# Kernel optimization log

Measured on AMD Instinct MI355X. Metric: run time of the kernel, lower is better.

The kernel has to match this reference:

```python
import jax, jax.numpy as jnp
import numpy as np

B, S, H, D = 4, 2048, 12, 64
HIDDEN = H * D  # 768
WINDOW = 64     # config.local_attention // 2
ROPE_THETA = 10000.0  # local_rope_theta for sliding layers


def rotate_half(x):
    d = x.shape[-1] // 2
    return jnp.concatenate([-x[..., d:], x[..., :d]], axis=-1)


def setup_inputs() -> dict:
    key = jax.random.key(0)
    k1, k2, k3 = jax.random.split(key, 3)
    hidden_states = jax.random.normal(k1, (B, S, HIDDEN), dtype=jnp.float32)
    # RoPE tables (HF style): inv_freq over half dims, duplicated
    inv_freq = 1.0 / (ROPE_THETA ** (jnp.arange(0, D, 2, dtype=jnp.float32) / D))  # [D/2]
    pos = jnp.arange(S, dtype=jnp.float32)
    freqs = pos[:, None] * inv_freq[None, :]          # [S, D/2]
    emb = jnp.concatenate([freqs, freqs], axis=-1)    # [S, D]
    cos = jnp.broadcast_to(jnp.cos(emb)[None], (B, S, D))
    sin = jnp.broadcast_to(jnp.sin(emb)[None], (B, S, D))
    # sliding-window additive mask [B,1,S,S]
    idx = jnp.arange(S)
    allowed = jnp.abs(idx[:, None] - idx[None, :]) <= WINDOW
    neg = jnp.finfo(jnp.float32).min
    attention_mask = jnp.broadcast_to(
        jnp.where(allowed, 0.0, neg)[None, None], (B, 1, S, S)
    ).astype(jnp.float32)
    std = 0.02
    Wqkv_w = jax.random.normal(k2, (3 * HIDDEN, HIDDEN), dtype=jnp.float32) * std
    Wo_w = jax.random.normal(k3, (HIDDEN, HIDDEN), dtype=jnp.float32) * std
    return {"hidden_states": hidden_states, "cos": cos, "sin": sin,
            "attention_mask": attention_mask, "Wqkv_w": Wqkv_w, "Wo_w": Wo_w}


def reference(hidden_states, cos, sin, attention_mask, Wqkv_w, Wo_w):
    b, s, _ = hidden_states.shape
    scaling = D ** -0.5
    qkv = hidden_states @ Wqkv_w.T                       # [B,S,3*HIDDEN]
    qkv = qkv.reshape(b, s, 3, H, D)
    q = jnp.transpose(qkv[:, :, 0], (0, 2, 1, 3))        # [B,H,S,D]
    k = jnp.transpose(qkv[:, :, 1], (0, 2, 1, 3))
    v = jnp.transpose(qkv[:, :, 2], (0, 2, 1, 3))
    # RoPE with float32 intermediates (inputs already fp32 here)
    c = cos[:, None].astype(jnp.float32)                 # [B,1,S,D]
    sn = sin[:, None].astype(jnp.float32)
    qf, kf = q.astype(jnp.float32), k.astype(jnp.float32)
    q = (qf * c + rotate_half(qf) * sn).astype(q.dtype)
    k = (kf * c + rotate_half(kf) * sn).astype(k.dtype)
    # SDPA with explicit additive mask
    scores = jnp.einsum('bhqd,bhkd->bhqk', q, k) * scaling + attention_mask
    attn = jax.nn.softmax(scores, axis=-1)
    out = jnp.einsum('bhqk,bhkd->bhqd', attn, v)         # [B,H,S,D]
    out = jnp.transpose(out, (0, 2, 1, 3)).reshape(b, s, HIDDEN)
    return out @ Wo_w.T
```

## Files before the change

kernel.cpp:

```cpp
#include <hip/hip_runtime.h>
#include <math.h>


typedef __attribute__((ext_vector_type(8))) short short8;
typedef __attribute__((ext_vector_type(4))) float floatx4;

constexpr int kB = 4;
constexpr int kS = 2048;
constexpr int kH = 12;
constexpr int kD = 64;
constexpr int kHidden = 768;
constexpr int kQKV = 3 * kHidden;

__device__ __forceinline__ unsigned short f2bf(float f) {
  union { float f; unsigned int u; } x; x.f = f;
  unsigned int r = (x.u + 0x7fffu + ((x.u >> 16) & 1u)) >> 16;
  return (unsigned short)r;
}

__global__ __launch_bounds__(256) void cvt_all(
    const float* __restrict__ h, const float* __restrict__ wqkv,
    const float* __restrict__ wo, unsigned short* __restrict__ hb,
    unsigned short* __restrict__ wqb, unsigned short* __restrict__ wob) {
  constexpr int n1 = kB * kS * kHidden / 4;
  constexpr int n2 = kQKV * kHidden / 4;
  constexpr int n3 = kHidden * kHidden / 4;
  int i = blockIdx.x * 256 + threadIdx.x;
  const float* src;
  unsigned short* dst;
  if (i < n1) {
    src = h; dst = hb;
  } else if (i < n1 + n2) {
    i -= n1; src = wqkv; dst = wqb;
  } else {
    i -= n1 + n2; if (i >= n3) return; src = wo; dst = wob;
  }
  const float4 v = ((const float4*)src)[i];
  ushort4 o;
  o.x = f2bf(v.x); o.y = f2bf(v.y); o.z = f2bf(v.z); o.w = f2bf(v.w);
  ((ushort4*)dst)[i] = o;
}

__device__ __forceinline__ void gload_lds16(const unsigned short* g, unsigned short* l) {
  __builtin_amdgcn_global_load_lds(
      (const __attribute__((address_space(1))) unsigned int*)g,
      (__attribute__((address_space(3))) unsigned int*)l, 16, 0, 0);
}

__global__ __launch_bounds__(512) void gemm_qkv(
    const unsigned short* __restrict__ A,
    const unsigned short* __restrict__ B,
    const float* __restrict__ cosp, const float* __restrict__ sinp,
    unsigned short* __restrict__ Qr, unsigned short* __restrict__ Kr,
    unsigned short* __restrict__ Vt) {
  constexpr int K = kHidden;
  constexpr int NP = 2 * (K / 64);
  __shared__ unsigned short SH[128 * 136];
  unsigned short* Ah0 = SH;
  unsigned short* Ah1 = SH + 4096;
  unsigned short* Bh0 = SH + 8192;
  unsigned short* Bh1 = SH + 12288;

  const int tid = threadIdx.x;
  const int lane = tid & 63;
  const int wave = tid >> 6;
  const int m0 = blockIdx.x * 128;
  const int n0 = blockIdx.y * 128;

  const int sc = wave * 64 + lane;
  const int srow = sc >> 2;
  const int sgc = ((sc & 3) ^ ((srow >> 1) & 3)) * 8;
  const int ldsOff = sc * 8;
  const unsigned short* gA0 = A + (size_t)(m0 + srow) * K + sgc;
  const unsigned short* gB0 = B + (size_t)(n0 + srow) * K + sgc;

  const int wm = wave >> 1, wn = wave & 1;
  const int mr = wm * 32 + (lane & 15);
  const int nr = wn * 64 + (lane & 15);
  const int kq = lane >> 4;

  int aOff[2], bOff[4];
#pragma unroll
  for (int i = 0; i < 2; i++) {
    const int r = mr + i * 16;
    aOff[i] = (r * 4 + (kq ^ ((r >> 1) & 3))) * 8;
  }
#pragma unroll
  for (int j = 0; j < 4; j++) {
    const int r = nr + j * 16;
    bOff[j] = (r * 4 + (kq ^ ((r >> 1) & 3))) * 8;
  }

  floatx4 acc[2][4];
#pragma unroll
  for (int i = 0; i < 2; i++)
#pragma unroll
    for (int j = 0; j < 4; j++) acc[i][j] = (floatx4)(0.f);

  gload_lds16(gA0, &Ah0[ldsOff]);
  gload_lds16(gB0, &Bh0[ldsOff]);

  for (int p = 0; p < NP; ++p) {
    if (p + 1 < NP) {
      const int kn = ((p + 1) >> 1) * 64 + ((p + 1) & 1) * 32;
      unsigned short* Ad = ((p + 1) & 1) ? Ah1 : Ah0;
      unsigned short* Bd = ((p + 1) & 1) ? Bh1 : Bh0;
      gload_lds16(gA0 + kn, &Ad[ldsOff]);
      gload_lds16(gB0 + kn, &Bd[ldsOff]);
      asm volatile("s_waitcnt vmcnt(2)" ::: "memory");
    } else {
      asm volatile("s_waitcnt vmcnt(0)" ::: "memory");
    }
    __builtin_amdgcn_s_barrier();
    __builtin_amdgcn_sched_barrier(0);
    const unsigned short* Asb = (p & 1) ? Ah1 : Ah0;
    const unsigned short* Bsb = (p & 1) ? Bh1 : Bh0;
    short8 af[2], bf[4];
#pragma unroll
    for (int i = 0; i < 2; i++) af[i] = *(const short8*)&Asb[aOff[i]];
#pragma unroll
    for (int j = 0; j < 4; j++) bf[j] = *(const short8*)&Bsb[bOff[j]];
#pragma unroll
    for (int i = 0; i < 2; i++)
#pragma unroll
      for (int j = 0; j < 4; j++)
        acc[i][j] = __builtin_amdgcn_mfma_f32_16x16x32_bf16(af[i], bf[j],
                                                            acc[i][j], 0, 0, 0);
    __builtin_amdgcn_sched_barrier(0);
    __builtin_amdgcn_s_barrier();
  }

  unsigned short (*Obuf)[136] = (unsigned short (*)[136])SH;

  const int region = n0 / kHidden;
  const int b = m0 >> 11, s0 = m0 & 2047;
  const int h0 = (n0 % kHidden) >> 6;
  const int rowL0 = wm * 32 + kq * 4;

  if (region == 2) {
#pragma unroll
    for (int i = 0; i < 2; i++)
#pragma unroll
      for (int r = 0; r < 4; r++) {
        const int rowL = rowL0 + i * 16 + r;
#pragma unroll
        for (int j = 0; j < 4; j++)
          Obuf[wn * 64 + j * 16 + (lane & 15)][rowL] = f2bf(acc[i][j][r]);
      }
    __syncthreads();
#pragma unroll
    for (int it = 0; it < 4; it++) {
      const int t = tid + it * 512;
      const int s8 = t & 15, rowc = t >> 4;
      const int hl = rowc >> 6, d = rowc & 63;
      *(short8*)(Vt + ((size_t)(b * kH + h0 + hl) * kD + d) * kS + s0 + s8 * 8) =
          *(const short8*)&Obuf[rowc][s8 * 8];
    }
  } else {
    unsigned short* dst = (region == 0) ? Qr : Kr;
    const float qscale = (region == 0) ? 0.125f : 1.f;
#pragma unroll
    for (int i = 0; i < 2; i++)
#pragma unroll
      for (int r = 0; r < 4; r++) {
        const int rowL = rowL0 + i * 16 + r;
        const int s = s0 + rowL;
        const float* cs = cosp + ((size_t)(b * kS + s)) * kD;
        const float* sns = sinp + ((size_t)(b * kS + s)) * kD;
#pragma unroll
        for (int jp = 0; jp < 2; jp++) {
          const int colL = wn * 64 + jp * 16 + (lane & 15);
          const int d = colL & 63;
          const float c = cs[d], sn = sns[d];
          const float xlo = acc[i][jp][r], xhi = acc[i][jp + 2][r];
          Obuf[rowL][colL]      = f2bf((xlo * c - xhi * sn) * qscale);
          Obuf[rowL][colL + 32] = f2bf((xhi * c + xlo * sn) * qscale);
        }
      }
    __syncthreads();
#pragma unroll
    for (int it = 0; it < 4; it++) {
      const int t = tid + it * 512;
      const int d8 = t & 7, sl = (t >> 3) & 127, hl = t >> 10;
      *(short8*)(dst + ((size_t)(b * kH + h0 + hl) * kS + s0 + sl) * kD + d8 * 8) =
          *(const short8*)&Obuf[sl][hl * 64 + d8 * 8];
    }
  }
}

__global__ __launch_bounds__(256) void gemm_bf16_nt(
    const unsigned short* __restrict__ A, const unsigned short* __restrict__ B,
    float* __restrict__ C, int M, int N, int K) {
  __shared__ unsigned short SH[4 * 4096];
  unsigned short* Ah0 = SH;
  unsigned short* Ah1 = SH + 4096;
  unsigned short* Bh0 = SH + 8192;
  unsigned short* Bh1 = SH + 12288;

  const int tid = threadIdx.x;
  const int lane = tid & 63;
  const int wave = tid >> 6;
  const int m0 = blockIdx.x * 128;
  const int n0 = blockIdx.y * 128;
  const int NP = 2 * (K / 64);

  int ldsOff[2];
  const unsigned short* gA0[2];
  const unsigned short* gB0[2];
#pragma unroll
  for (int t = 0; t < 2; t++) {
    const int sc = wave * 128 + t * 64 + lane;
    const int srow = sc >> 2;
    const int sgc = ((sc & 3) ^ ((srow >> 1) & 3)) * 8;
    ldsOff[t] = sc * 8;
    gA0[t] = A + (size_t)(m0 + srow) * K + sgc;
    gB0[t] = B + (size_t)(n0 + srow) * K + sgc;
  }

  const int wm = wave >> 1, wn = wave & 1;
  const int mr = wm * 64 + (lane & 15);
  const int nr = wn * 64 + (lane & 15);
  const int kq = lane >> 4;

  int aOff[4], bOff[4];
#pragma unroll
  for (int i = 0; i < 4; i++) {
    const int ra = mr + i * 16;
    aOff[i] = (ra * 4 + (kq ^ ((ra >> 1) & 3))) * 8;
    const int rb = nr + i * 16;
    bOff[i] = (rb * 4 + (kq ^ ((rb >> 1) & 3))) * 8;
  }

  floatx4 acc[4][4];
#pragma unroll
  for (int i = 0; i < 4; i++)
#pragma unroll
    for (int j = 0; j < 4; j++) acc[i][j] = (floatx4)(0.f);

#pragma unroll
  for (int t = 0; t < 2; t++) {
    gload_lds16(gA0[t], &Ah0[ldsOff[t]]);
    gload_lds16(gB0[t], &Bh0[ldsOff[t]]);
  }

  for (int p = 0; p < NP; ++p) {
    if (p + 1 < NP) {
      const int kn = ((p + 1) >> 1) * 64 + ((p + 1) & 1) * 32;
      unsigned short* Ad = ((p + 1) & 1) ? Ah1 : Ah0;
      unsigned short* Bd = ((p + 1) & 1) ? Bh1 : Bh0;
#pragma unroll
      for (int t = 0; t < 2; t++) {
        gload_lds16(gA0[t] + kn, &Ad[ldsOff[t]]);
        gload_lds16(gB0[t] + kn, &Bd[ldsOff[t]]);
      }
      asm volatile("s_waitcnt vmcnt(4)" ::: "memory");
    } else {
      asm volatile("s_waitcnt vmcnt(0)" ::: "memory");
    }
    __builtin_amdgcn_s_barrier();
    __builtin_amdgcn_sched_barrier(0);
    const unsigned short* Asb = (p & 1) ? Ah1 : Ah0;
    const unsigned short* Bsb = (p & 1) ? Bh1 : Bh0;
    short8 af[4], bf[4];
#pragma unroll
    for (int i = 0; i < 4; i++) {
      af[i] = *(const short8*)&Asb[aOff[i]];
      bf[i] = *(const short8*)&Bsb[bOff[i]];
    }
#pragma unroll
    for (int i = 0; i < 4; i++)
#pragma unroll
      for (int j = 0; j < 4; j++)
        acc[i][j] = __builtin_amdgcn_mfma_f32_16x16x32_bf16(af[i], bf[j],
                                                            acc[i][j], 0, 0, 0);
    __builtin_amdgcn_sched_barrier(0);
    __builtin_amdgcn_s_barrier();
  }

  const int crow = m0 + wm * 64 + kq * 4;
  const int ccol = n0 + wn * 64 + (lane & 15);
#pragma unroll
  for (int i = 0; i < 4; i++)
#pragma unroll
    for (int r = 0; r < 4; r++) {
      float* cp = C + (size_t)(crow + i * 16 + r) * N + ccol;
#pragma unroll
      for (int j = 0; j < 4; j++) cp[j * 16] = acc[i][j][r];
    }
}

constexpr int AQT = 32;

__global__ __launch_bounds__(256) void attn_v3(
    const unsigned short* __restrict__ Qr, const unsigned short* __restrict__ Kr,
    const unsigned short* __restrict__ Vt, unsigned short* __restrict__ out) {
  __shared__ unsigned short Pfrag[2][5][64][8];
  __shared__ float Ssum[2][AQT];

  const int tid = threadIdx.x;
  const int lane = tid & 63;
  const int wave = tid >> 6;
  const int quad = lane >> 4;
  const int l15 = lane & 15;
  const int qbase = blockIdx.x * AQT;
  const int h = blockIdx.y, b = blockIdx.z;
  const int bh = b * kH + h;
  const int kbase = qbase - 64;
  const int tq = wave >> 1;
  const int kh = wave & 1;

  short8 vf[2][5];
  {
    const unsigned short* vbase = Vt + (size_t)bh * kD * kS;
#pragma unroll
    for (int nt = 0; nt < 2; nt++) {
      const unsigned short* vrow = vbase + (size_t)(kh * 32 + nt * 16 + l15) * kS;
#pragma unroll
      for (int kk = 0; kk < 5; kk++) {
        int s0 = kbase + kk * 32 + quad * 8;
        s0 = min(max(s0, 0), kS - 8);
        vf[nt][kk] = *(const short8*)(vrow + s0);
      }
    }
  }

  const unsigned short* qsrc =
      Qr + ((size_t)bh * kS + qbase + tq * 16 + l15) * kD + quad * 8;
  const short8 a0 = *(const short8*)qsrc;
  const short8 a1 = *(const short8*)(qsrc + 32);

  floatx4 acc[5];
  const unsigned short* ksrc = Kr + (size_t)bh * kS * kD;
#pragma unroll
  for (int g = 0; g < 5; g++) {
    int row = kbase + (kh * 5 + g) * 16 + l15;
    row = min(max(row, 0), kS - 1);
    const unsigned short* kp = ksrc + (size_t)row * kD + quad * 8;
    const short8 b0 = *(const short8*)kp;
    const short8 b1 = *(const short8*)(kp + 32);
    floatx4 z = (floatx4)(0.f);
    z = __builtin_amdgcn_mfma_f32_16x16x32_bf16(a0, b0, z, 0, 0, 0);
    z = __builtin_amdgcn_mfma_f32_16x16x32_bf16(a1, b1, z, 0, 0, 0);
    acc[g] = z;
  }

#pragma unroll
  for (int r = 0; r < 4; r++) {
    const int q = tq * 16 + quad * 4 + r;
    float s = 0.f;
#pragma unroll
    for (int g = 0; g < 5; g++) {
      const int key = (kh * 5 + g) * 16 + l15;
      const int kg_ = kbase + key;
      const bool valid = (key >= q) && (key <= q + 128) && (kg_ >= 0) && (kg_ < kS);
      const float e = valid ? __expf(acc[g][r]) : 0.f;
      s += e;
      Pfrag[tq][key >> 5][((key >> 3) & 3) * 16 + quad * 4 + r][key & 7] = f2bf(e);
    }
#pragma unroll
    for (int off = 1; off < 16; off <<= 1) s += __shfl_xor(s, off, 64);
    if (l15 == 0) Ssum[kh][q] = s;
  }
  __syncthreads();

  floatx4 o0 = (floatx4)(0.f), o1 = (floatx4)(0.f);
#pragma unroll
  for (int kk = 0; kk < 5; kk++) {
    const short8 pa = *(const short8*)&Pfrag[tq][kk][lane][0];
    o0 = __builtin_amdgcn_mfma_f32_16x16x32_bf16(pa, vf[0][kk], o0, 0, 0, 0);
    o1 = __builtin_amdgcn_mfma_f32_16x16x32_bf16(pa, vf[1][kk], o1, 0, 0, 0);
  }

#pragma unroll
  for (int r = 0; r < 4; r++) {
    const int q = tq * 16 + quad * 4 + r;
    const float inv = 1.f / (Ssum[0][q] + Ssum[1][q]);
    unsigned short* op =
        out + ((size_t)(b * kS + qbase + q)) * kHidden + h * kD + kh * 32 + l15;
    op[0] = f2bf(o0[r] * inv);
    op[16] = f2bf(o1[r] * inv);
  }
}

extern "C" void kernel_launch(void* const* d_in, const int* in_sizes, int n_in,
                              void* d_out, int out_size, void* d_ws,
                              size_t ws_size, hipStream_t stream) {
  const float* hidden = (const float*)d_in[0];
  const float* cosp = (const float*)d_in[1];
  const float* sinp = (const float*)d_in[2];
  const float* wqkv = (const float*)d_in[4];
  const float* wo = (const float*)d_in[5];
  float* out = (float*)d_out;

  const int M = kB * kS;
  const size_t szH = (size_t)M * kHidden;

  unsigned short* hbf = (unsigned short*)d_ws;
  unsigned short* wqkvbf = hbf + szH;
  unsigned short* wobf = wqkvbf + (size_t)kQKV * kHidden;
  unsigned short* attnbf = wobf + (size_t)kHidden * kHidden;
  unsigned short* Qrb = attnbf + szH;
  unsigned short* Krb = Qrb + szH;
  unsigned short* Vtb = Krb + szH;

  const int ncvt = (M * kHidden + kQKV * kHidden + kHidden * kHidden) / 4;
  cvt_all<<<(ncvt + 255) / 256, 256, 0, stream>>>(hidden, wqkv, wo, hbf,
                                                  wqkvbf, wobf);

  dim3 g1(M / 128, kQKV / 128);
  gemm_qkv<<<g1, 512, 0, stream>>>(hbf, wqkvbf, cosp, sinp, Qrb, Krb, Vtb);

  dim3 ga(kS / AQT, kH, kB);
  attn_v3<<<ga, 256, 0, stream>>>(Qrb, Krb, Vtb, attnbf);

  dim3 g2(M / 128, kHidden / 128);
  gemm_bf16_nt<<<g2, 256, 0, stream>>>(attnbf, wobf, out, M, kHidden, kHidden);
}
```

Baseline: 215.3 us.

## Enlarge QKV GEMM tile to 256 rows and stage attention output through LDS

The QKV projection GEMM now computes 256x128 tiles per block, so each wave holds a 4x4 accumulator grid and each B tile is reused across more rows. The epilogue runs in two 128-row halves so it fits the existing LDS buffer. The K-offset computation in both GEMMs is simplified to a linear step. The attention kernel now writes its output through shared memory and stores 16-byte vectors instead of scattered 2-byte stores. The larger tile halves the grid and raises register pressure, which could reduce occupancy.

```diff
diff --git a/kernel.cpp b/kernel.cpp
--- a/kernel.cpp
+++ b/kernel.cpp
@@ -47,7 +47,7 @@
       (__attribute__((address_space(3))) unsigned int*)l, 16, 0, 0);
 }
 
-__global__ __launch_bounds__(512) void gemm_qkv(
+__global__ __launch_bounds__(512, 4) void gemm_qkv(
     const unsigned short* __restrict__ A,
     const unsigned short* __restrict__ B,
     const float* __restrict__ cosp, const float* __restrict__ sinp,
@@ -55,59 +55,71 @@
     unsigned short* __restrict__ Vt) {
   constexpr int K = kHidden;
   constexpr int NP = 2 * (K / 64);
-  __shared__ unsigned short SH[128 * 136];
+  __shared__ unsigned short SH[24576];
   unsigned short* Ah0 = SH;
-  unsigned short* Ah1 = SH + 4096;
-  unsigned short* Bh0 = SH + 8192;
-  unsigned short* Bh1 = SH + 12288;
+  unsigned short* Ah1 = SH + 8192;
+  unsigned short* Bh0 = SH + 16384;
+  unsigned short* Bh1 = SH + 20480;
 
   const int tid = threadIdx.x;
   const int lane = tid & 63;
   const int wave = tid >> 6;
-  const int m0 = blockIdx.x * 128;
+  const int l15 = lane & 15;
+  const int m0 = blockIdx.x * 256;
   const int n0 = blockIdx.y * 128;
 
-  const int sc = wave * 64 + lane;
-  const int srow = sc >> 2;
-  const int sgc = ((sc & 3) ^ ((srow >> 1) & 3)) * 8;
-  const int ldsOff = sc * 8;
-  const unsigned short* gA0 = A + (size_t)(m0 + srow) * K + sgc;
-  const unsigned short* gB0 = B + (size_t)(n0 + srow) * K + sgc;
+  int ldsA[2];
+  const unsigned short* gA[2];
+#pragma unroll
+  for (int t = 0; t < 2; t++) {
+    const int sc = (wave * 2 + t) * 64 + lane;
+    const int srow = sc >> 2;
+    const int sgc = ((sc & 3) ^ ((srow >> 1) & 3)) * 8;
+    ldsA[t] = sc * 8;
+    gA[t] = A + (size_t)(m0 + srow) * K + sgc;
+  }
+  const int scB = wave * 64 + lane;
+  const int ldsB = scB * 8;
+  const unsigned short* gB;
+  {
+    const int srow = scB >> 2;
+    const int sgc = ((scB & 3) ^ ((srow >> 1) & 3)) * 8;
+    gB = B + (size_t)(n0 + srow) * K + sgc;
+  }
 
   const int wm = wave >> 1, wn = wave & 1;
-  const int mr = wm * 32 + (lane & 15);
-  const int nr = wn * 64 + (lane & 15);
+  const int mr = wm * 64 + l15;
+  const int nr = wn * 64 + l15;
   const int kq = lane >> 4;
 
-  int aOff[2], bOff[4];
-#pragma unroll
-  for (int i = 0; i < 2; i++) {
-    const int r = mr + i * 16;
-    aOff[i] = (r * 4 + (kq ^ ((r >> 1) & 3))) * 8;
-  }
-#pragma unroll
-  for (int j = 0; j < 4; j++) {
-    const int r = nr + j * 16;
-    bOff[j] = (r * 4 + (kq ^ ((r >> 1) & 3))) * 8;
-  }
-
-  floatx4 acc[2][4];
-#pragma unroll
-  for (int i = 0; i < 2; i++)
+  int aOff[4], bOff[4];
+#pragma unroll
+  for (int i = 0; i < 4; i++) {
+    const int ra = mr + i * 16;
+    aOff[i] = (ra * 4 + (kq ^ ((ra >> 1) & 3))) * 8;
+    const int rb = nr + i * 16;
+    bOff[i] = (rb * 4 + (kq ^ ((rb >> 1) & 3))) * 8;
+  }
+
+  floatx4 acc[4][4];
+#pragma unroll
+  for (int i = 0; i < 4; i++)
 #pragma unroll
     for (int j = 0; j < 4; j++) acc[i][j] = (floatx4)(0.f);
 
-  gload_lds16(gA0, &Ah0[ldsOff]);
-  gload_lds16(gB0, &Bh0[ldsOff]);
+  gload_lds16(gA[0], &Ah0[ldsA[0]]);
+  gload_lds16(gA[1], &Ah0[ldsA[1]]);
+  gload_lds16(gB, &Bh0[ldsB]);
 
   for (int p = 0; p < NP; ++p) {
     if (p + 1 < NP) {
-      const int kn = ((p + 1) >> 1) * 64 + ((p + 1) & 1) * 32;
+      const int kn = (p + 1) * 32;
       unsigned short* Ad = ((p + 1) & 1) ? Ah1 : Ah0;
       unsigned short* Bd = ((p + 1) & 1) ? Bh1 : Bh0;
-      gload_lds16(gA0 + kn, &Ad[ldsOff]);
-      gload_lds16(gB0 + kn, &Bd[ldsOff]);
-      asm volatile("s_waitcnt vmcnt(2)" ::: "memory");
+      gload_lds16(gA[0] + kn, &Ad[ldsA[0]]);
+      gload_lds16(gA[1] + kn, &Ad[ldsA[1]]);
+      gload_lds16(gB + kn, &Bd[ldsB]);
+      asm volatile("s_waitcnt vmcnt(3)" ::: "memory");
     } else {
       asm volatile("s_waitcnt vmcnt(0)" ::: "memory");
     }
@@ -115,13 +127,14 @@
     __builtin_amdgcn_sched_barrier(0);
     const unsigned short* Asb = (p & 1) ? Ah1 : Ah0;
     const unsigned short* Bsb = (p & 1) ? Bh1 : Bh0;
-    short8 af[2], bf[4];
-#pragma unroll
-    for (int i = 0; i < 2; i++) af[i] = *(const short8*)&Asb[aOff[i]];
-#pragma unroll
-    for (int j = 0; j < 4; j++) bf[j] = *(const short8*)&Bsb[bOff[j]];
-#pragma unroll
-    for (int i = 0; i < 2; i++)
+    short8 af[4], bf[4];
+#pragma unroll
+    for (int i = 0; i < 4; i++) {
+      af[i] = *(const short8*)&Asb[aOff[i]];
+      bf[i] = *(const short8*)&Bsb[bOff[i]];
+    }
+#pragma unroll
+    for (int i = 0; i < 4; i++)
 #pragma unroll
       for (int j = 0; j < 4; j++)
         acc[i][j] = __builtin_amdgcn_mfma_f32_16x16x32_bf16(af[i], bf[j],
@@ -135,55 +148,64 @@
   const int region = n0 / kHidden;
   const int b = m0 >> 11, s0 = m0 & 2047;
   const int h0 = (n0 % kHidden) >> 6;
-  const int rowL0 = wm * 32 + kq * 4;
-
-  if (region == 2) {
-#pragma unroll
-    for (int i = 0; i < 2; i++)
-#pragma unroll
-      for (int r = 0; r < 4; r++) {
-        const int rowL = rowL0 + i * 16 + r;
-#pragma unroll
-        for (int j = 0; j < 4; j++)
-          Obuf[wn * 64 + j * 16 + (lane & 15)][rowL] = f2bf(acc[i][j][r]);
+  const int rwBase = (wm & 1) * 64 + kq * 4;
+  const int myHalf = wm >> 1;
+
+  for (int half = 0; half < 2; half++) {
+    __syncthreads();
+    if (myHalf == half) {
+      if (region == 2) {
+#pragma unroll
+        for (int i = 0; i < 4; i++)
+#pragma unroll
+          for (int r = 0; r < 4; r++) {
+            const int rw = rwBase + i * 16 + r;
+#pragma unroll
+            for (int j = 0; j < 4; j++)
+              Obuf[wn * 64 + j * 16 + l15][rw] = f2bf(acc[i][j][r]);
+          }
+      } else {
+        const float qscale = (region == 0) ? 0.125f : 1.f;
+#pragma unroll
+        for (int i = 0; i < 4; i++)
+#pragma unroll
+          for (int r = 0; r < 4; r++) {
+            const int rw = rwBase + i * 16 + r;
+            const int s = s0 + half * 128 + rw;
+            const float* cs = cosp + ((size_t)(b * kS + s)) * kD;
+            const float* sns = sinp + ((size_t)(b * kS + s)) * kD;
+#pragma unroll
+            for (int jp = 0; jp < 2; jp++) {
+              const int colL = wn * 64 + jp * 16 + l15;
+              const int d = colL & 63;
+              const float c = cs[d], sn = sns[d];
+              const float xlo = acc[i][jp][r], xhi = acc[i][jp + 2][r];
+              Obuf[rw][colL]      = f2bf((xlo * c - xhi * sn) * qscale);
+              Obuf[rw][colL + 32] = f2bf((xhi * c + xlo * sn) * qscale);
+            }
+          }
       }
+    }
     __syncthreads();
-#pragma unroll
-    for (int it = 0; it < 4; it++) {
-      const int t = tid + it * 512;
-      const int s8 = t & 15, rowc = t >> 4;
-      const int hl = rowc >> 6, d = rowc & 63;
-      *(short8*)(Vt + ((size_t)(b * kH + h0 + hl) * kD + d) * kS + s0 + s8 * 8) =
-          *(const short8*)&Obuf[rowc][s8 * 8];
-    }
-  } else {
-    unsigned short* dst = (region == 0) ? Qr : Kr;
-    const float qscale = (region == 0) ? 0.125f : 1.f;
-#pragma unroll
-    for (int i = 0; i < 2; i++)
-#pragma unroll
-      for (int r = 0; r < 4; r++) {
-        const int rowL = rowL0 + i * 16 + r;
-        const int s = s0 + rowL;
-        const float* cs = cosp + ((size_t)(b * kS + s)) * kD;
-        const float* sns = sinp + ((size_t)(b * kS + s)) * kD;
-#pragma unroll
-        for (int jp = 0; jp < 2; jp++) {
-          const int colL = wn * 64 + jp * 16 + (lane & 15);
-          const int d = colL & 63;
-          const float c = cs[d], sn = sns[d];
-          const float xlo = acc[i][jp][r], xhi = acc[i][jp + 2][r];
-          Obuf[rowL][colL]      = f2bf((xlo * c - xhi * sn) * qscale);
-          Obuf[rowL][colL + 32] = f2bf((xhi * c + xlo * sn) * qscale);
-        }
+    const int sOff = s0 + half * 128;
+    if (region == 2) {
+#pragma unroll
+      for (int it = 0; it < 4; it++) {
+        const int t = tid + it * 512;
+        const int s8 = t & 15, rowc = t >> 4;
+        const int hl = rowc >> 6, d = rowc & 63;
+        *(short8*)(Vt + ((size_t)(b * kH + h0 + hl) * kD + d) * kS + sOff + s8 * 8) =
+            *(const short8*)&Obuf[rowc][s8 * 8];
       }
-    __syncthreads();
-#pragma unroll
-    for (int it = 0; it < 4; it++) {
-      const int t = tid + it * 512;
-      const int d8 = t & 7, sl = (t >> 3) & 127, hl = t >> 10;
-      *(short8*)(dst + ((size_t)(b * kH + h0 + hl) * kS + s0 + sl) * kD + d8 * 8) =
-          *(const short8*)&Obuf[sl][hl * 64 + d8 * 8];
+    } else {
+      unsigned short* dst = (region == 0) ? Qr : Kr;
+#pragma unroll
+      for (int it = 0; it < 4; it++) {
+        const int t = tid + it * 512;
+        const int d8 = t & 7, sl = (t >> 3) & 127, hl = t >> 10;
+        *(short8*)(dst + ((size_t)(b * kH + h0 + hl) * kS + sOff + sl) * kD + d8 * 8) =
+            *(const short8*)&Obuf[sl][hl * 64 + d8 * 8];
+      }
     }
   }
 }
@@ -245,7 +267,7 @@
 
   for (int p = 0; p < NP; ++p) {
     if (p + 1 < NP) {
-      const int kn = ((p + 1) >> 1) * 64 + ((p + 1) & 1) * 32;
+      const int kn = (p + 1) * 32;
       unsigned short* Ad = ((p + 1) & 1) ? Ah1 : Ah0;
       unsigned short* Bd = ((p + 1) & 1) ? Bh1 : Bh0;
 #pragma unroll
@@ -371,14 +393,20 @@
     o1 = __builtin_amdgcn_mfma_f32_16x16x32_bf16(pa, vf[1][kk], o1, 0, 0, 0);
   }
 
+  __syncthreads();
+  unsigned short (*Ob)[68] = (unsigned short (*)[68])Pfrag;
 #pragma unroll
   for (int r = 0; r < 4; r++) {
     const int q = tq * 16 + quad * 4 + r;
     const float inv = 1.f / (Ssum[0][q] + Ssum[1][q]);
-    unsigned short* op =
-        out + ((size_t)(b * kS + qbase + q)) * kHidden + h * kD + kh * 32 + l15;
-    op[0] = f2bf(o0[r] * inv);
-    op[16] = f2bf(o1[r] * inv);
+    Ob[q][kh * 32 + l15] = f2bf(o0[r] * inv);
+    Ob[q][kh * 32 + 16 + l15] = f2bf(o1[r] * inv);
+  }
+  __syncthreads();
+  {
+    const int q = tid >> 3, d8 = tid & 7;
+    *(short8*)(out + ((size_t)(b * kS + qbase + q)) * kHidden + h * kD + d8 * 8) =
+        *(const short8*)&Ob[q][d8 * 8];
   }
 }
 
@@ -407,7 +435,7 @@
   cvt_all<<<(ncvt + 255) / 256, 256, 0, stream>>>(hidden, wqkv, wo, hbf,
                                                   wqkvbf, wobf);
 
-  dim3 g1(M / 128, kQKV / 128);
+  dim3 g1(M / 256, kQKV / 128);
   gemm_qkv<<<g1, 512, 0, stream>>>(hbf, wqkvbf, cosp, sinp, Qrb, Krb, Vtb);
 
   dim3 ga(kS / AQT, kH, kB);
```

Result: slower. 284.9 us (+32.3%).

## Use single-buffered 64-wide K tiles in GEMM and stage attention output via LDS

Applied to the files above, without the earlier changes.

The GEMM drops its double-buffered 32-wide K pipeline, which used manual vmcnt waits, in favour of a single LDS buffer holding 64-wide K tiles with an XOR swizzle and __syncthreads around each tile. This halves the number of barrier rounds but gives up the overlap of global loads with MFMA work. The attention kernel now writes its normalized bf16 output into LDS (reusing Pfrag) and then stores it as coalesced 16-byte vectors instead of scattered 2-byte stores. The LDS staging adds two extra block barriers.

```diff
diff --git a/kernel.cpp b/kernel.cpp
--- a/kernel.cpp
+++ b/kernel.cpp
@@ -191,30 +191,26 @@
 __global__ __launch_bounds__(256) void gemm_bf16_nt(
     const unsigned short* __restrict__ A, const unsigned short* __restrict__ B,
     float* __restrict__ C, int M, int N, int K) {
-  __shared__ unsigned short SH[4 * 4096];
-  unsigned short* Ah0 = SH;
-  unsigned short* Ah1 = SH + 4096;
-  unsigned short* Bh0 = SH + 8192;
-  unsigned short* Bh1 = SH + 12288;
+  __shared__ unsigned short As[128 * 64];
+  __shared__ unsigned short Bs[128 * 64];
 
   const int tid = threadIdx.x;
   const int lane = tid & 63;
   const int wave = tid >> 6;
   const int m0 = blockIdx.x * 128;
   const int n0 = blockIdx.y * 128;
-  const int NP = 2 * (K / 64);
-
-  int ldsOff[2];
-  const unsigned short* gA0[2];
-  const unsigned short* gB0[2];
-#pragma unroll
-  for (int t = 0; t < 2; t++) {
-    const int sc = wave * 128 + t * 64 + lane;
-    const int srow = sc >> 2;
-    const int sgc = ((sc & 3) ^ ((srow >> 1) & 3)) * 8;
-    ldsOff[t] = sc * 8;
-    gA0[t] = A + (size_t)(m0 + srow) * K + sgc;
-    gB0[t] = B + (size_t)(n0 + srow) * K + sgc;
+
+  int ldsS[4];
+  const unsigned short* gA[4];
+  const unsigned short* gB[4];
+#pragma unroll
+  for (int t = 0; t < 4; t++) {
+    const int ci = (wave * 4 + t) * 64 + lane;
+    const int row = ci >> 3;
+    const int c = (ci & 7) ^ (row & 7);
+    ldsS[t] = ci * 8;
+    gA[t] = A + (size_t)(m0 + row) * K + c * 8;
+    gB[t] = B + (size_t)(n0 + row) * K + c * 8;
   }
 
   const int wm = wave >> 1, wn = wave & 1;
@@ -222,59 +218,35 @@
   const int nr = wn * 64 + (lane & 15);
   const int kq = lane >> 4;
 
-  int aOff[4], bOff[4];
-#pragma unroll
-  for (int i = 0; i < 4; i++) {
-    const int ra = mr + i * 16;
-    aOff[i] = (ra * 4 + (kq ^ ((ra >> 1) & 3))) * 8;
-    const int rb = nr + i * 16;
-    bOff[i] = (rb * 4 + (kq ^ ((rb >> 1) & 3))) * 8;
-  }
-
   floatx4 acc[4][4];
 #pragma unroll
   for (int i = 0; i < 4; i++)
 #pragma unroll
     for (int j = 0; j < 4; j++) acc[i][j] = (floatx4)(0.f);
 
-#pragma unroll
-  for (int t = 0; t < 2; t++) {
-    gload_lds16(gA0[t], &Ah0[ldsOff[t]]);
-    gload_lds16(gB0[t], &Bh0[ldsOff[t]]);
-  }
-
-  for (int p = 0; p < NP; ++p) {
-    if (p + 1 < NP) {
-      const int kn = ((p + 1) >> 1) * 64 + ((p + 1) & 1) * 32;
-      unsigned short* Ad = ((p + 1) & 1) ? Ah1 : Ah0;
-      unsigned short* Bd = ((p + 1) & 1) ? Bh1 : Bh0;
-#pragma unroll
-      for (int t = 0; t < 2; t++) {
-        gload_lds16(gA0[t] + kn, &Ad[ldsOff[t]]);
-        gload_lds16(gB0[t] + kn, &Bd[ldsOff[t]]);
+  for (int k0 = 0; k0 < K; k0 += 64) {
+    if (k0) __syncthreads();
+#pragma unroll
+    for (int t = 0; t < 4; t++) {
+      gload_lds16(gA[t] + k0, &As[ldsS[t]]);
+      gload_lds16(gB[t] + k0, &Bs[ldsS[t]]);
+    }
+    __syncthreads();
+#pragma unroll
+    for (int s = 0; s < 2; s++) {
+      short8 af[4], bf[4];
+#pragma unroll
+      for (int i = 0; i < 4; i++) {
+        af[i] = *(const short8*)&As[(mr + i * 16) * 64 + (((s * 4 + kq) ^ (mr & 7)) * 8)];
+        bf[i] = *(const short8*)&Bs[(nr + i * 16) * 64 + (((s * 4 + kq) ^ (nr & 7)) * 8)];
       }
-      asm volatile("s_waitcnt vmcnt(4)" ::: "memory");
-    } else {
-      asm volatile("s_waitcnt vmcnt(0)" ::: "memory");
-    }
-    __builtin_amdgcn_s_barrier();
-    __builtin_amdgcn_sched_barrier(0);
-    const unsigned short* Asb = (p & 1) ? Ah1 : Ah0;
-    const unsigned short* Bsb = (p & 1) ? Bh1 : Bh0;
-    short8 af[4], bf[4];
-#pragma unroll
-    for (int i = 0; i < 4; i++) {
-      af[i] = *(const short8*)&Asb[aOff[i]];
-      bf[i] = *(const short8*)&Bsb[bOff[i]];
-    }
-#pragma unroll
-    for (int i = 0; i < 4; i++)
-#pragma unroll
-      for (int j = 0; j < 4; j++)
-        acc[i][j] = __builtin_amdgcn_mfma_f32_16x16x32_bf16(af[i], bf[j],
-                                                            acc[i][j], 0, 0, 0);
-    __builtin_amdgcn_sched_barrier(0);
-    __builtin_amdgcn_s_barrier();
+#pragma unroll
+      for (int i = 0; i < 4; i++)
+#pragma unroll
+        for (int j = 0; j < 4; j++)
+          acc[i][j] = __builtin_amdgcn_mfma_f32_16x16x32_bf16(af[i], bf[j],
+                                                              acc[i][j], 0, 0, 0);
+    }
   }
 
   const int crow = m0 + wm * 64 + kq * 4;
@@ -371,14 +343,20 @@
     o1 = __builtin_amdgcn_mfma_f32_16x16x32_bf16(pa, vf[1][kk], o1, 0, 0, 0);
   }
 
+  __syncthreads();
+  unsigned short (*Ob)[68] = (unsigned short (*)[68])Pfrag;
 #pragma unroll
   for (int r = 0; r < 4; r++) {
     const int q = tq * 16 + quad * 4 + r;
     const float inv = 1.f / (Ssum[0][q] + Ssum[1][q]);
-    unsigned short* op =
-        out + ((size_t)(b * kS + qbase + q)) * kHidden + h * kD + kh * 32 + l15;
-    op[0] = f2bf(o0[r] * inv);
-    op[16] = f2bf(o1[r] * inv);
+    Ob[q][kh * 32 + l15] = f2bf(o0[r] * inv);
+    Ob[q][kh * 32 + 16 + l15] = f2bf(o1[r] * inv);
+  }
+  __syncthreads();
+  {
+    const int q = tid >> 3, d8 = tid & 7;
+    *(short8*)(out + ((size_t)(b * kS + qbase + q)) * kHidden + h * kD + d8 * 8) =
+        *(const short8*)&Ob[q][d8 * 8];
   }
 }
 
```

Measured after the change: 214.7 us. About the same (-0.3%).
